# Performance work log

Measured on AMD Instinct MI355X. Metric: run time of the kernel, lower is better.

## Reference

```python
import jax, jax.numpy as jnp
import numpy as np

B, T, C = 4, 2048, 1024
NH = 16
HS = C // NH


def setup_inputs() -> dict:
    key = jax.random.key(0)
    k1, k2, k3, k4, k5 = jax.random.split(key, 5)
    scale = 1.0 / np.sqrt(C)
    return {
        "x": jax.random.normal(k1, (B, T, C), dtype=jnp.float32),
        "Wk": jax.random.normal(k2, (C, C), dtype=jnp.float32) * scale,
        "Wq": jax.random.normal(k3, (C, C), dtype=jnp.float32) * scale,
        "Wv": jax.random.normal(k4, (C, C), dtype=jnp.float32) * scale,
        "Wp": jax.random.normal(k5, (C, C), dtype=jnp.float32) * scale,
    }


def reference(x, Wk, Wq, Wv, Wp):
    b, t, c = x.shape
    # projections (nn.Linear with bias=False computes x @ W.T; weights here are
    # stored so that x @ W is equivalent -- same math, random init either way)
    k = (x @ Wk).reshape(b, t, NH, HS).transpose(0, 2, 1, 3)  # [B,H,T,hs]
    q = (x @ Wq).reshape(b, t, NH, HS).transpose(0, 2, 1, 3)
    v = (x @ Wv).reshape(b, t, NH, HS).transpose(0, 2, 1, 3)
    att = jnp.einsum("bhqd,bhkd->bhqk", q, k) / jnp.sqrt(jnp.float32(HS))
    causal = jnp.tril(jnp.ones((t, t), dtype=bool))
    att = jnp.where(causal[None, None, :, :], att, -jnp.inf)
    att = jax.nn.softmax(att, axis=-1)
    y = jnp.einsum("bhqk,bhkd->bhqd", att, v)  # [B,H,T,hs]
    y = y.transpose(0, 2, 1, 3).reshape(b, t, c)
    return y @ Wp
```

## Files before the change

### kernel.cpp

```cpp
#include <hip/hip_runtime.h>
#include <cstddef>
#include <cstdint>


namespace {

typedef unsigned short u16;
typedef unsigned int u32;
typedef __attribute__((ext_vector_type(8))) short s8v;
typedef __attribute__((ext_vector_type(4))) short s4v;
typedef __attribute__((ext_vector_type(4))) float f4v;

constexpr int Bn = 4, Tn = 2048, Cn = 1024;
constexpr int KVB = 128;
constexpr int NT128 = Tn / 128;
constexpr float QSCALE = 0.125f * 1.44269504f;

__device__ __forceinline__ u16 bfc(float f) {
  return __builtin_bit_cast(u16, (__bf16)f);
}

__device__ __forceinline__ float ex2(float x) {
#if __has_builtin(__builtin_amdgcn_exp2f)
  return __builtin_amdgcn_exp2f(x);
#else
  return exp2f(x);
#endif
}

__device__ __forceinline__ f4v mfma16(s8v a, s8v b, f4v c) {
  return __builtin_amdgcn_mfma_f32_16x16x32_bf16(a, b, c, 0, 0, 0);
}

__device__ __forceinline__ f4v mfma16k16(s4v a, s4v b, f4v c) {
#if __has_builtin(__builtin_amdgcn_mfma_f32_16x16x16bf16_1k)
  return __builtin_amdgcn_mfma_f32_16x16x16bf16_1k(a, b, c, 0, 0, 0);
#else
  f4v d = c;
  asm("v_mfma_f32_16x16x16_bf16 %0, %1, %2, %0" : "+v"(d) : "v"(a), "v"(b));
  return d;
#endif
}

typedef __attribute__((address_space(1))) const u32 gas_u32;
typedef __attribute__((address_space(3))) u32 las_u32;
__device__ __forceinline__ void gl_lds16(const void* g, void* l) {
  __builtin_amdgcn_global_load_lds((gas_u32*)g, (las_u32*)l, 16, 0, 0);
}

__global__ __launch_bounds__(256) void prep(
    const float* __restrict__ x, u16* __restrict__ xb,
    const float* __restrict__ w0, const float* __restrict__ w1,
    const float* __restrict__ w2, const float* __restrict__ w3,
    u16* __restrict__ o0, u16* __restrict__ o1, u16* __restrict__ o2,
    u16* __restrict__ o3) {
  __shared__ float Tsh[64][65];
  const int bid = blockIdx.x;
  const int tid = threadIdx.x;
  if (bid < 4096) {
    const size_t i = ((size_t)bid * 256 + tid) * 8;
    const float4 a = *(const float4*)(x + i);
    const float4 b = *(const float4*)(x + i + 4);
    alignas(16) u16 t[8] = {bfc(a.x), bfc(a.y), bfc(a.z), bfc(a.w),
                            bfc(b.x), bfc(b.y), bfc(b.z), bfc(b.w)};
    *(s8v*)(xb + i) = *(const s8v*)t;
    return;
  }
  const int idx = bid - 4096;
  const int wz = idx >> 8, wy = (idx >> 4) & 15, wx = idx & 15;
  const float* W;
  u16* O;
  switch (wz) {
    case 0: W = w0; O = o0; break;
    case 1: W = w1; O = o1; break;
    case 2: W = w2; O = o2; break;
    default: W = w3; O = o3; break;
  }
  const int n0 = wx * 64, k0 = wy * 64;
  {
    const int rk = tid >> 2, c0 = (tid & 3) * 16;
#pragma unroll
    for (int u = 0; u < 4; ++u) {
      const float4 v = *(const float4*)&W[(size_t)(k0 + rk) * Cn + n0 + c0 + u * 4];
      Tsh[rk][c0 + u * 4 + 0] = v.x;
      Tsh[rk][c0 + u * 4 + 1] = v.y;
      Tsh[rk][c0 + u * 4 + 2] = v.z;
      Tsh[rk][c0 + u * 4 + 3] = v.w;
    }
  }
  __syncthreads();
  {
    const int rn = tid >> 2, ck0 = (tid & 3) * 16;
    alignas(16) u16 t[16];
#pragma unroll
    for (int u = 0; u < 16; ++u) t[u] = bfc(Tsh[ck0 + u][rn]);
    *(s8v*)&O[(size_t)(n0 + rn) * Cn + k0 + ck0] = *(const s8v*)&t[0];
    *(s8v*)&O[(size_t)(n0 + rn) * Cn + k0 + ck0 + 8] = *(const s8v*)&t[8];
  }
}

template <int OUT_MODE>
__device__ __forceinline__ void gemm_body(const u16* __restrict__ A,
                                          const u16* __restrict__ Bt,
                                          void* __restrict__ Cout, int bm,
                                          int bn, u16* As, u16* Bs) {
  const int N = Cn, K = Cn;
  const int tid = threadIdx.x;
  const int l = tid & 63, w = tid >> 6;
  const int lr = l & 15, lh = l >> 4;
  const int wm = (w >> 1) * 64, wn = (w & 1) * 64;
  const u16* Ab = A + (size_t)(bm * 128) * K;
  const u16* Bb = Bt + (size_t)(bn * 128) * K;
  const int sw = lr & 7;
  f4v acc[4][4] = {};
  for (int k0 = 0; k0 < K; k0 += 64) {
    __syncthreads();
#pragma unroll
    for (int i = 0; i < 4; ++i) {
      const int s = tid + 256 * i;
      const int r = s >> 3, c = s & 7;
      gl_lds16(Ab + (size_t)r * K + k0 + ((c ^ (r & 7)) * 8), &As[s * 8]);
    }
#pragma unroll
    for (int i = 0; i < 4; ++i) {
      const int s = tid + 256 * i;
      const int r = s >> 3, c = s & 7;
      gl_lds16(Bb + (size_t)r * K + k0 + ((c ^ (r & 7)) * 8), &Bs[s * 8]);
    }
    __syncthreads();
#pragma unroll
    for (int half = 0; half < 2; ++half) {
      s8v af[4], bfr[4];
#pragma unroll
      for (int i = 0; i < 4; ++i)
        af[i] = *(const s8v*)&As[(wm + i * 16 + lr) * 64 +
                                 (((half * 4 + lh) ^ sw) * 8)];
#pragma unroll
      for (int j = 0; j < 4; ++j)
        bfr[j] = *(const s8v*)&Bs[(wn + j * 16 + lr) * 64 +
                                  (((half * 4 + lh) ^ sw) * 8)];
      __builtin_amdgcn_s_setprio(1);
#pragma unroll
      for (int i = 0; i < 4; ++i)
#pragma unroll
        for (int j = 0; j < 4; ++j)
          acc[i][j] = mfma16(af[i], bfr[j], acc[i][j]);
      __builtin_amdgcn_s_setprio(0);
    }
  }
  if (OUT_MODE == 2) {
    float* Cf = (float*)Cout;
#pragma unroll
    for (int i = 0; i < 4; ++i) {
      const int row = bm * 128 + wm + i * 16 + lh * 4;
#pragma unroll
      for (int j = 0; j < 4; ++j) {
        const int col = bn * 128 + wn + j * 16 + lr;
#pragma unroll
        for (int r = 0; r < 4; ++r)
          Cf[(size_t)(row + r) * N + col] = acc[i][j][r];
      }
    }
  } else if (OUT_MODE == 0 || OUT_MODE == 3) {
    u16* Cb = (u16*)Cout;
    const float sc = (OUT_MODE == 3) ? QSCALE : 1.0f;
#pragma unroll
    for (int i = 0; i < 4; ++i) {
      const int row = bm * 128 + wm + i * 16 + lh * 4;
#pragma unroll
      for (int j = 0; j < 4; ++j) {
        const int col = bn * 128 + wn + j * 16 + lr;
#pragma unroll
        for (int r = 0; r < 4; ++r)
          Cb[(size_t)(row + r) * N + col] = bfc(acc[i][j][r] * sc);
      }
    }
  } else {
    u16* Vt = (u16*)Cout;
#pragma unroll
    for (int i = 0; i < 4; ++i) {
      const int row0 = bm * 128 + wm + i * 16 + lh * 4;
      const int bq = row0 >> 11;
      const int t0g = row0 & 2047;
      const int tau = t0g & 127;
      const int taup = ((tau >> 5) << 5) | (((tau >> 2) & 3) << 3) |
                       (((tau >> 4) & 1) << 2);
      const int t0p = (t0g & ~127) | taup;
#pragma unroll
      for (int j = 0; j < 4; ++j) {
        const int col = bn * 128 + wn + j * 16 + lr;
        const int hh = col >> 6, dd = col & 63;
        alignas(8) u16 t4[4];
#pragma unroll
        for (int r = 0; r < 4; ++r) t4[r] = bfc(acc[i][j][r]);
        *(s4v*)&Vt[((size_t)((bq * 16 + hh) * 64 + dd)) * Tn + t0p] =
            *(const s4v*)t4;
      }
    }
  }
}

__global__ __launch_bounds__(256) void gemm_qkv(
    const u16* __restrict__ A, const u16* __restrict__ btq,
    const u16* __restrict__ btk, const u16* __restrict__ btv,
    u16* __restrict__ qb, u16* __restrict__ kb, u16* __restrict__ vt) {
  __shared__ __align__(16) u16 As[8192], Bs[8192];
  const int bid = blockIdx.x;
  const int xcd = bid & 7, j = bid >> 3;
  const int bm = xcd * 8 + (j & 7);
  const int combo = j >> 3;
  const int which = combo >> 3, bn = combo & 7;
  if (which == 0)
    gemm_body<3>(A, btq, qb, bm, bn, As, Bs);
  else if (which == 1)
    gemm_body<0>(A, btk, kb, bm, bn, As, Bs);
  else
    gemm_body<1>(A, btv, vt, bm, bn, As, Bs);
}

template <int OUT_MODE>
__global__ __launch_bounds__(256) void gemm_bt(const u16* __restrict__ A,
                                               const u16* __restrict__ Bt,
                                               void* __restrict__ Cout) {
  __shared__ __align__(16) u16 As[8192], Bs[8192];
  const int bid = blockIdx.x;
  const int xcd = bid & 7, j = bid >> 3;
  const int bm = xcd * 8 + (j & 7);
  const int bn = j >> 3;
  gemm_body<OUT_MODE>(A, Bt, Cout, bm, bn, As, Bs);
}

__device__ __forceinline__ void stage_kv(const u16* __restrict__ kgb,
                                         const u16* __restrict__ vtb,
                                         u16* __restrict__ Kb,
                                         u16* __restrict__ Vb, int k0,
                                         int tid) {
#pragma unroll
  for (int is = 0; is < 2; ++is) {
    const int slot = is * 512 + tid;
    const int row = slot >> 3, ch = slot & 7;
    gl_lds16(kgb + (size_t)(k0 + row) * Cn + ((ch ^ (row & 7)) * 8),
             &Kb[slot * 8]);
  }
#pragma unroll
  for (int is = 0; is < 2; ++is) {
    const int slot = is * 512 + tid;
    const int d = slot >> 4, ch = slot & 15;
    gl_lds16(vtb + (size_t)d * Tn + k0 + ((ch ^ (d & 7)) * 8), &Vb[slot * 8]);
  }
}

__device__ __forceinline__ void attn_step(const s8v (&aq)[2],
                                          const u16* __restrict__ Ks,
                                          const u16* __restrict__ Vs, int kb0,
                                          int kb1, const int (&vch)[4], int ln,
                                          int lh, bool diag, int k0, int qg,
                                          float& m_i, float& l_i, f4v* o) {
  f4v s[8] = {};
  __builtin_amdgcn_s_setprio(1);
#pragma unroll
  for (int n = 0; n < 8; ++n) {
    const s8v bk0 = *(const s8v*)&Ks[kb0 + n * 1024];
    const s8v bk1 = *(const s8v*)&Ks[kb1 + n * 1024];
    s[n] = mfma16(bk0, aq[0], s[n]);
    s[n] = mfma16(bk1, aq[1], s[n]);
  }
  __builtin_amdgcn_s_setprio(0);
  float rm = -1e30f;
  if (diag) {
#pragma unroll
    for (int n = 0; n < 8; ++n)
#pragma unroll
      for (int r = 0; r < 4; ++r) {
        float x = s[n][r];
        if (k0 + n * 16 + lh * 4 + r > qg) x = -1e30f;
        s[n][r] = x;
        rm = fmaxf(rm, x);
      }
  } else {
#pragma unroll
    for (int n = 0; n < 8; ++n)
      rm = fmaxf(rm, fmaxf(fmaxf(s[n][0], s[n][1]), fmaxf(s[n][2], s[n][3])));
  }
  if (!__all(rm <= m_i + 11.5f)) {
    float rr = fmaxf(rm, __shfl_xor(rm, 16));
    rr = fmaxf(rr, __shfl_xor(rr, 32));
    const float mnew = fmaxf(m_i, rr);
    const float al = ex2(m_i - mnew);
    m_i = mnew;
    l_i *= al;
#pragma unroll
    for (int r = 0; r < 4; ++r) {
      const float ar = __shfl(al, (ln & 48) | (lh * 4 + r));
#pragma unroll
      for (int n2 = 0; n2 < 4; ++n2) o[n2][r] *= ar;
    }
  }
  s4v pa[8];
  float rs = 0.f;
#pragma unroll
  for (int n = 0; n < 8; ++n) {
    const float p0 = ex2(s[n][0] - m_i);
    const float p1 = ex2(s[n][1] - m_i);
    const float p2 = ex2(s[n][2] - m_i);
    const float p3 = ex2(s[n][3] - m_i);
    rs += (p0 + p1) + (p2 + p3);
    pa[n] = (s4v){(short)bfc(p0), (short)bfc(p1), (short)bfc(p2),
                  (short)bfc(p3)};
  }
  l_i += rs;
  __builtin_amdgcn_s_setprio(1);
#pragma unroll
  for (int n2 = 0; n2 < 4; ++n2) {
#pragma unroll
    for (int p = 0; p < 4; ++p) {
      const s8v vv = *(const s8v*)&Vs[vch[p] + n2 * 2048];
      const s4v lo = {vv[0], vv[1], vv[2], vv[3]};
      const s4v hi = {vv[4], vv[5], vv[6], vv[7]};
      o[n2] = mfma16k16(pa[2 * p], lo, o[n2]);
      o[n2] = mfma16k16(pa[2 * p + 1], hi, o[n2]);
    }
  }
  __builtin_amdgcn_s_setprio(0);
}

__global__ __launch_bounds__(512) void attn_big(const u16* __restrict__ qg,
                                                const u16* __restrict__ kg,
                                                const u16* __restrict__ vtg,
                                                u16* __restrict__ yg) {
  __shared__ __align__(16) u16 Ks0[KVB * 64], Ks1[KVB * 64];
  __shared__ __align__(16) u16 Vs0[64 * KVB], Vs1[64 * KVB];
  const int tid = threadIdx.x;
  const int ln = tid & 63, w = tid >> 6;
  const int lr = ln & 15, lh = ln >> 4;
  const int bid = blockIdx.x;
  const int wg = (bid & 7) * 64 + (bid >> 3);
  const int bh = wg >> 3, xp = wg & 7;
  const int b = bh >> 4, h = bh & 15;
  const int tL = xp, tH = NT128 - 1 - xp;
  const int q0L = tL * 128, q0H = tH * 128;
  const u16* kgb = kg + (size_t)(b * Tn) * Cn + h * 64;
  const u16* vtb = vtg + (size_t)(bh * 64) * Tn;
  const int kb0 = lr * 64 + ((lh) ^ (lr & 7)) * 8;
  const int kb1 = lr * 64 + ((4 + lh) ^ (lr & 7)) * 8;
  int vch[4];
#pragma unroll
  for (int p = 0; p < 4; ++p)
    vch[p] = lr * 128 + ((p * 4 + lh) ^ (lr & 7)) * 8;
  s8v aqL[2], aqH[2];
  {
    const int row = w * 16 + lr;
#pragma unroll
    for (int kd = 0; kd < 2; ++kd) {
      aqL[kd] = *(const s8v*)&qg[(size_t)(b * Tn + q0L + row) * Cn + h * 64 +
                                 kd * 32 + lh * 8];
      aqH[kd] = *(const s8v*)&qg[(size_t)(b * Tn + q0H + row) * Cn + h * 64 +
                                 kd * 32 + lh * 8];
    }
  }
  const int qgH = q0H + w * 16 + lr;
  const int qgL = q0L + w * 16 + lr;
  float mL = -1e30f, lL = 0.f, mH = -1e30f, lH = 0.f;
  f4v oL[4] = {}, oH[4] = {};
  stage_kv(kgb, vtb, Ks0, Vs0, 0, tid);
  __syncthreads();
  for (int kt = 0; kt <= tH; ++kt) {
    const bool cur = kt & 1;
    const u16* Kb = cur ? Ks1 : Ks0;
    const u16* Vb = cur ? Vs1 : Vs0;
    if (kt < tH)
      stage_kv(kgb, vtb, cur ? Ks0 : Ks1, cur ? Vs0 : Vs1, (kt + 1) * KVB,
               tid);
    attn_step(aqH, Kb, Vb, kb0, kb1, vch, ln, lh, kt == tH, kt * KVB, qgH, mH,
              lH, oH);
    if (kt <= tL)
      attn_step(aqL, Kb, Vb, kb0, kb1, vch, ln, lh, kt == tL, kt * KVB, qgL,
                mL, lL, oL);
    __syncthreads();
  }
  {
    float ls = lH;
    ls += __shfl_xor(ls, 16);
    ls += __shfl_xor(ls, 32);
    const float linv = 1.0f / ls;
#pragma unroll
    for (int r = 0; r < 4; ++r) {
      const float iv = __shfl(linv, (ln & 48) | (lh * 4 + r));
      const int row = q0H + w * 16 + lh * 4 + r;
#pragma unroll
      for (int n2 = 0; n2 < 4; ++n2)
        yg[(size_t)(b * Tn + row) * Cn + h * 64 + n2 * 16 + lr] =
            bfc(oH[n2][r] * iv);
    }
  }
  {
    float ls = lL;
    ls += __shfl_xor(ls, 16);
    ls += __shfl_xor(ls, 32);
    const float linv = 1.0f / ls;
#pragma unroll
    for (int r = 0; r < 4; ++r) {
      const float iv = __shfl(linv, (ln & 48) | (lh * 4 + r));
      const int row = q0L + w * 16 + lh * 4 + r;
#pragma unroll
      for (int n2 = 0; n2 < 4; ++n2)
        yg[(size_t)(b * Tn + row) * Cn + h * 64 + n2 * 16 + lr] =
            bfc(oL[n2][r] * iv);
    }
  }
}

}

extern "C" void kernel_launch(void* const* d_in, const int* in_sizes, int n_in,
                              void* d_out, int out_size, void* d_ws,
                              size_t ws_size, hipStream_t stream) {
  (void)in_sizes; (void)n_in; (void)out_size; (void)ws_size;
  const float* x = (const float*)d_in[0];
  const float* Wk = (const float*)d_in[1];
  const float* Wq = (const float*)d_in[2];
  const float* Wv = (const float*)d_in[3];
  const float* Wp = (const float*)d_in[4];
  float* out = (float*)d_out;
  char* ws = (char*)d_ws;

  u16* xb = (u16*)(ws);
  u16* wqt = (u16*)(ws + 16777216);
  u16* wkt = (u16*)(ws + 18874368);
  u16* wvt = (u16*)(ws + 20971520);
  u16* wpt = (u16*)(ws + 23068672);
  u16* qb = (u16*)(ws + 25165824);
  u16* kb = (u16*)(ws + 41943040);
  u16* vt = (u16*)(ws + 58720256);
  u16* yb = (u16*)(ws + 75497472);

  prep<<<dim3(5120), dim3(256), 0, stream>>>(x, xb, Wq, Wk, Wv, Wp, wqt, wkt,
                                             wvt, wpt);
  gemm_qkv<<<dim3(1536), dim3(256), 0, stream>>>(xb, wqt, wkt, wvt, qb, kb,
                                                 vt);
  attn_big<<<dim3(512), dim3(512), 0, stream>>>(qb, kb, vt, yb);
  gemm_bt<2><<<dim3(512), dim3(256), 0, stream>>>(yb, wpt, out);
}
```

Before: 168.5 us.

## Rewrite projection GEMMs as 256x128 tiles with triple-buffered async LDS pipeline

The projection GEMM body now uses 512-thread blocks computing 256x128 output tiles. Global-to-LDS loads run through a three-stage ring buffer, with the next-next K tile staged while the current one is consumed, and explicit vmcnt waits and barriers replace the sync-load-sync pattern. The aim is to hide global load latency behind MFMA work and raise reuse per tile. In exchange the blocks use much more LDS (144 KB) and the grid has half as many blocks, which can lower occupancy and tail balance.

```diff
diff --git a/kernel.cpp b/kernel.cpp
--- a/kernel.cpp
+++ b/kernel.cpp
@@ -100,86 +100,118 @@
 }
 
 template <int OUT_MODE>
-__device__ __forceinline__ void gemm_body(const u16* __restrict__ A,
-                                          const u16* __restrict__ Bt,
-                                          void* __restrict__ Cout, int bm,
-                                          int bn, u16* As, u16* Bs) {
-  const int N = Cn, K = Cn;
+__device__ __forceinline__ void gemm8p(const u16* __restrict__ A,
+                                       const u16* __restrict__ Bt,
+                                       void* __restrict__ Cout, int bm,
+                                       int bn, u16* lds) {
+  const int K = Cn;
   const int tid = threadIdx.x;
   const int l = tid & 63, w = tid >> 6;
   const int lr = l & 15, lh = l >> 4;
-  const int wm = (w >> 1) * 64, wn = (w & 1) * 64;
-  const u16* Ab = A + (size_t)(bm * 128) * K;
+  const int wm = (w >> 2) * 128, wn = (w & 3) * 32;
+  const int sw = lr & 7;
+  const u16* Ab = A + (size_t)(bm * 256) * K;
   const u16* Bb = Bt + (size_t)(bn * 128) * K;
-  const int sw = lr & 7;
-  f4v acc[4][4] = {};
-  for (int k0 = 0; k0 < K; k0 += 64) {
-    __syncthreads();
-#pragma unroll
-    for (int i = 0; i < 4; ++i) {
-      const int s = tid + 256 * i;
+  f4v acc[8][2] = {};
+
+  auto stage_unit = [&](int buf, int kt, int u) {
+    u16* dst = lds + buf * 24576 + (u == 2 ? 16384 : u * 8192);
+    const u16* src = (u == 2) ? Bb : (Ab + (size_t)(u * 128) * K);
+    {
+      const int r = tid >> 3, c = tid & 7;
+      gl_lds16(src + (size_t)r * K + kt * 64 + ((c ^ (r & 7)) * 8),
+               dst + (size_t)tid * 8);
+    }
+    {
+      const int s = tid + 512;
       const int r = s >> 3, c = s & 7;
-      gl_lds16(Ab + (size_t)r * K + k0 + ((c ^ (r & 7)) * 8), &As[s * 8]);
-    }
-#pragma unroll
-    for (int i = 0; i < 4; ++i) {
-      const int s = tid + 256 * i;
-      const int r = s >> 3, c = s & 7;
-      gl_lds16(Bb + (size_t)r * K + k0 + ((c ^ (r & 7)) * 8), &Bs[s * 8]);
-    }
-    __syncthreads();
-#pragma unroll
-    for (int half = 0; half < 2; ++half) {
-      s8v af[4], bfr[4];
+      gl_lds16(src + (size_t)r * K + kt * 64 + ((c ^ (r & 7)) * 8),
+               dst + (size_t)s * 8);
+    }
+  };
+
+  stage_unit(0, 0, 0);
+  stage_unit(0, 0, 1);
+  stage_unit(0, 0, 2);
+  stage_unit(1, 1, 0);
+  stage_unit(1, 1, 1);
+  stage_unit(1, 1, 2);
+  asm volatile("s_waitcnt vmcnt(6)" ::: "memory");
+  __builtin_amdgcn_s_barrier();
+
+  const int NK = K / 64;
+  for (int j = 0; j < NK; ++j) {
+    const int cb = j % 3;
+    const int nb = (j + 2) % 3;
+    const bool more = (j + 2) < NK;
+    const u16* Ac = lds + cb * 24576;
+    const u16* Bc = Ac + 16384;
+#pragma unroll
+    for (int p = 0; p < 4; ++p) {
+      const int mh = p & 1, kh = p >> 1;
+      s8v av[4], bv[2];
 #pragma unroll
       for (int i = 0; i < 4; ++i)
-        af[i] = *(const s8v*)&As[(wm + i * 16 + lr) * 64 +
-                                 (((half * 4 + lh) ^ sw) * 8)];
-#pragma unroll
-      for (int j = 0; j < 4; ++j)
-        bfr[j] = *(const s8v*)&Bs[(wn + j * 16 + lr) * 64 +
-                                  (((half * 4 + lh) ^ sw) * 8)];
+        av[i] = *(const s8v*)&Ac[(wm + mh * 64 + i * 16 + lr) * 64 +
+                                 (((kh * 4 + lh) ^ sw) * 8)];
+#pragma unroll
+      for (int jj = 0; jj < 2; ++jj)
+        bv[jj] = *(const s8v*)&Bc[(wn + jj * 16 + lr) * 64 +
+                                  (((kh * 4 + lh) ^ sw) * 8)];
+      if (p < 3) {
+        if (more) stage_unit(nb, j + 2, p);
+      } else {
+        if (more)
+          asm volatile("s_waitcnt vmcnt(6)" ::: "memory");
+        else
+          asm volatile("s_waitcnt vmcnt(0)" ::: "memory");
+      }
+      __builtin_amdgcn_s_barrier();
+      asm volatile("s_waitcnt lgkmcnt(0)" ::: "memory");
+      __builtin_amdgcn_sched_barrier(0);
       __builtin_amdgcn_s_setprio(1);
 #pragma unroll
       for (int i = 0; i < 4; ++i)
 #pragma unroll
-        for (int j = 0; j < 4; ++j)
-          acc[i][j] = mfma16(af[i], bfr[j], acc[i][j]);
+        for (int jj = 0; jj < 2; ++jj)
+          acc[mh * 4 + i][jj] = mfma16(av[i], bv[jj], acc[mh * 4 + i][jj]);
       __builtin_amdgcn_s_setprio(0);
-    }
-  }
+      __builtin_amdgcn_s_barrier();
+    }
+  }
+
   if (OUT_MODE == 2) {
     float* Cf = (float*)Cout;
 #pragma unroll
-    for (int i = 0; i < 4; ++i) {
-      const int row = bm * 128 + wm + i * 16 + lh * 4;
-#pragma unroll
-      for (int j = 0; j < 4; ++j) {
-        const int col = bn * 128 + wn + j * 16 + lr;
+    for (int i = 0; i < 8; ++i) {
+      const int row = bm * 256 + wm + i * 16 + lh * 4;
+#pragma unroll
+      for (int jj = 0; jj < 2; ++jj) {
+        const int col = bn * 128 + wn + jj * 16 + lr;
 #pragma unroll
         for (int r = 0; r < 4; ++r)
-          Cf[(size_t)(row + r) * N + col] = acc[i][j][r];
+          Cf[(size_t)(row + r) * Cn + col] = acc[i][jj][r];
       }
     }
   } else if (OUT_MODE == 0 || OUT_MODE == 3) {
     u16* Cb = (u16*)Cout;
     const float sc = (OUT_MODE == 3) ? QSCALE : 1.0f;
 #pragma unroll
-    for (int i = 0; i < 4; ++i) {
-      const int row = bm * 128 + wm + i * 16 + lh * 4;
-#pragma unroll
-      for (int j = 0; j < 4; ++j) {
-        const int col = bn * 128 + wn + j * 16 + lr;
+    for (int i = 0; i < 8; ++i) {
+      const int row = bm * 256 + wm + i * 16 + lh * 4;
+#pragma unroll
+      for (int jj = 0; jj < 2; ++jj) {
+        const int col = bn * 128 + wn + jj * 16 + lr;
 #pragma unroll
         for (int r = 0; r < 4; ++r)
-          Cb[(size_t)(row + r) * N + col] = bfc(acc[i][j][r] * sc);
+          Cb[(size_t)(row + r) * Cn + col] = bfc(acc[i][jj][r] * sc);
       }
     }
   } else {
     u16* Vt = (u16*)Cout;
 #pragma unroll
-    for (int i = 0; i < 4; ++i) {
-      const int row0 = bm * 128 + wm + i * 16 + lh * 4;
+    for (int i = 0; i < 8; ++i) {
+      const int row0 = bm * 256 + wm + i * 16 + lh * 4;
       const int bq = row0 >> 11;
       const int t0g = row0 & 2047;
       const int tau = t0g & 127;
@@ -187,12 +219,12 @@
                        (((tau >> 4) & 1) << 2);
       const int t0p = (t0g & ~127) | taup;
 #pragma unroll
-      for (int j = 0; j < 4; ++j) {
-        const int col = bn * 128 + wn + j * 16 + lr;
+      for (int jj = 0; jj < 2; ++jj) {
+        const int col = bn * 128 + wn + jj * 16 + lr;
         const int hh = col >> 6, dd = col & 63;
         alignas(8) u16 t4[4];
 #pragma unroll
-        for (int r = 0; r < 4; ++r) t4[r] = bfc(acc[i][j][r]);
+        for (int r = 0; r < 4; ++r) t4[r] = bfc(acc[i][jj][r]);
         *(s4v*)&Vt[((size_t)((bq * 16 + hh) * 64 + dd)) * Tn + t0p] =
             *(const s4v*)t4;
       }
@@ -200,34 +232,34 @@
   }
 }
 
-__global__ __launch_bounds__(256) void gemm_qkv(
+__global__ __launch_bounds__(512) void gemm_qkv(
     const u16* __restrict__ A, const u16* __restrict__ btq,
     const u16* __restrict__ btk, const u16* __restrict__ btv,
     u16* __restrict__ qb, u16* __restrict__ kb, u16* __restrict__ vt) {
-  __shared__ __align__(16) u16 As[8192], Bs[8192];
+  __shared__ __align__(16) u16 lds[73728];
   const int bid = blockIdx.x;
-  const int xcd = bid & 7, j = bid >> 3;
-  const int bm = xcd * 8 + (j & 7);
-  const int combo = j >> 3;
+  const int xcd = bid & 7, loc = bid >> 3;
+  const int bm = xcd * 4 + (loc & 3);
+  const int combo = loc >> 2;
   const int which = combo >> 3, bn = combo & 7;
   if (which == 0)
-    gemm_body<3>(A, btq, qb, bm, bn, As, Bs);
+    gemm8p<3>(A, btq, qb, bm, bn, lds);
   else if (which == 1)
-    gemm_body<0>(A, btk, kb, bm, bn, As, Bs);
+    gemm8p<0>(A, btk, kb, bm, bn, lds);
   else
-    gemm_body<1>(A, btv, vt, bm, bn, As, Bs);
+    gemm8p<1>(A, btv, vt, bm, bn, lds);
 }
 
 template <int OUT_MODE>
-__global__ __launch_bounds__(256) void gemm_bt(const u16* __restrict__ A,
+__global__ __launch_bounds__(512) void gemm_bt(const u16* __restrict__ A,
                                                const u16* __restrict__ Bt,
                                                void* __restrict__ Cout) {
-  __shared__ __align__(16) u16 As[8192], Bs[8192];
+  __shared__ __align__(16) u16 lds[73728];
   const int bid = blockIdx.x;
-  const int xcd = bid & 7, j = bid >> 3;
-  const int bm = xcd * 8 + (j & 7);
-  const int bn = j >> 3;
-  gemm_body<OUT_MODE>(A, Bt, Cout, bm, bn, As, Bs);
+  const int xcd = bid & 7, loc = bid >> 3;
+  const int bm = xcd * 4 + (loc & 3);
+  const int bn = loc >> 2;
+  gemm8p<OUT_MODE>(A, Bt, Cout, bm, bn, lds);
 }
 
 __device__ __forceinline__ void stage_kv(const u16* __restrict__ kgb,
@@ -436,8 +468,8 @@
 
   prep<<<dim3(5120), dim3(256), 0, stream>>>(x, xb, Wq, Wk, Wv, Wp, wqt, wkt,
                                              wvt, wpt);
-  gemm_qkv<<<dim3(1536), dim3(256), 0, stream>>>(xb, wqt, wkt, wvt, qb, kb,
-                                                 vt);
+  gemm_qkv<<<dim3(768), dim3(512), 0, stream>>>(xb, wqt, wkt, wvt, qb, kb,
+                                                vt);
   attn_big<<<dim3(512), dim3(512), 0, stream>>>(qb, kb, vt, yb);
-  gemm_bt<2><<<dim3(512), dim3(256), 0, stream>>>(yb, wpt, out);
-}
+  gemm_bt<2><<<dim3(256), dim3(512), 0, stream>>>(yb, wpt, out);
+}
```

Result: no change. 168.8 us, median of 2 (+0.2%).
